# Performance work log

Measured on AMD Instinct MI355X. Metric: run time of the kernel, lower is better.

Reference implementation:

```python
import jax, jax.numpy as jnp
import numpy as np

GH = 256       # GRU hidden size
VOCAB = 1000
MAX_EP = 150
NPREV = NCURR = NNEXT = 64


def _gru_scan(emb, h0, wih, whh, bih, bhh):
    # torch nn.GRU single-layer math, scanned over the token axis
    H = h0.shape[0]
    def step(h, x_t):
        gi = wih @ x_t + bih            # [3H]
        gh = whh @ h + bhh              # [3H]
        r = jax.nn.sigmoid(gi[:H] + gh[:H])
        z = jax.nn.sigmoid(gi[H:2 * H] + gh[H:2 * H])
        n = jnp.tanh(gi[2 * H:] + r * gh[2 * H:])
        hn = (1.0 - z) * n + z * h
        return hn, hn
    _, hs = jax.lax.scan(step, h0, emb)
    return hs                            # [L, H]


def _conv(x, w, b, s):
    y = jax.lax.conv_general_dilated(x, w, (s, s), 'VALID',
                                     dimension_numbers=('NCHW', 'OIHW', 'NCHW'))
    return y + b[None, :, None, None]


def setup_inputs():
    key = jax.random.key(0)
    ks = jax.random.split(key, 48)
    f32 = jnp.float32
    def W(i, shape, s=0.05):
        return (jax.random.normal(ks[i], shape) * s).astype(f32)
    inp = dict(
        x=jax.random.normal(ks[0], (1, 3, 124, 124), f32),
        hx=jax.random.normal(ks[1], (1, 256), f32),
        cx=jax.random.normal(ks[2], (1, 256), f32),
        conv1_w=W(3, (128, 3, 8, 8)), conv1_b=jnp.zeros((128,), f32),
        conv2_w=W(4, (64, 128, 4, 4)), conv2_b=jnp.zeros((64,), f32),
        conv3_w=W(5, (64, 64, 4, 4)), conv3_b=jnp.zeros((64,), f32),
        emb_w=W(6, (VOCAB, 32), 1.0),
        gru_f_wih=W(7, (3 * GH, 32)), gru_f_whh=W(8, (3 * GH, GH)),
        gru_f_bih=jnp.zeros((3 * GH,), f32), gru_f_bhh=jnp.zeros((3 * GH,), f32),
        gru_b_wih=W(9, (3 * GH, 32)), gru_b_whh=W(10, (3 * GH, GH)),
        gru_b_bih=jnp.zeros((3 * GH,), f32), gru_b_bhh=jnp.zeros((3 * GH,), f32),
        time_emb_w=W(11, (MAX_EP + 1, 32), 1.0),
        temp_emb_w=W(12, (2, 32), 1.0),
        img_emb_w=W(13, (256, 64 * 6 * 6)), img_emb_b=jnp.zeros((256,), f32),
        attn_key_w=W(14, (256, 256 * 3)), attn_key_b=jnp.zeros((256,), f32),
        bilinear_A=W(15, (1, 256, 544)), bilinear_b=jnp.zeros((1,), f32),
        reduce_w=W(16, (128, 544)), reduce_b=jnp.zeros((128,), f32),
        gate_w=W(17, (64, 640)), gate_b=jnp.zeros((64,), f32),
        lin_w=W(18, (256, 64 * 6 * 6)), lin_b=jnp.zeros((256,), f32),
        lstm_wih=W(19, (1024, 256)), lstm_whh=W(20, (1024, 256)),
        lstm_bih=jnp.zeros((1024,), f32), lstm_bhh=jnp.zeros((1024,), f32),
        critic_w=W(21, (1, 288)), critic_b=jnp.zeros((1,), f32),
        actor_w=W(22, (4, 288)), actor_b=jnp.zeros((4,), f32),
        prev_inst=jax.random.randint(ks[23], (1, NPREV), 0, VOCAB),
        curr_inst=jax.random.randint(ks[24], (1, NCURR), 0, VOCAB),
        next_inst=jax.random.randint(ks[25], (1, NNEXT), 0, VOCAB),
        tx=jax.random.randint(ks[26], (1,), 0, MAX_EP + 1),
    )
    return inp


def reference(x, hx, cx, conv1_w, conv1_b, conv2_w, conv2_b, conv3_w, conv3_b,
              emb_w, gru_f_wih, gru_f_whh, gru_f_bih, gru_f_bhh,
              gru_b_wih, gru_b_whh, gru_b_bih, gru_b_bhh,
              time_emb_w, temp_emb_w, img_emb_w, img_emb_b,
              attn_key_w, attn_key_b, bilinear_A, bilinear_b,
              reduce_w, reduce_b, gate_w, gate_b, lin_w, lin_b,
              lstm_wih, lstm_whh, lstm_bih, lstm_bhh,
              critic_w, critic_b, actor_w, actor_b,
              prev_inst, curr_inst, next_inst, tx):
    np_, nc, nn_ = prev_inst.shape[1], curr_inst.shape[1], next_inst.shape[1]
    all_inst = jnp.concatenate([prev_inst, curr_inst, next_inst], axis=1)[0]  # [L]
    L = all_inst.shape[0]

    # CNN encoder
    h = jax.nn.relu(_conv(x, conv1_w, conv1_b, 4))
    h = jax.nn.relu(_conv(h, conv2_w, conv2_b, 2))
    x_img = jax.nn.relu(_conv(h, conv3_w, conv3_b, 2))       # [1,64,6,6]

    # token-looped GRUs -> single lax.scan each (note: original runs gru_b
    # over the SAME forward order then reverses the hidden list; replicated)
    emb = emb_w[all_inst]                                    # [L,32]
    h0 = jnp.zeros((GH,), emb.dtype)
    hs_f = _gru_scan(emb, h0, gru_f_wih, gru_f_whh, gru_f_bih, gru_f_bhh)
    hs_b = _gru_scan(emb, h0, gru_b_wih, gru_b_whh, gru_b_bih, gru_b_bhh)[::-1]
    curr_instr_rep = jnp.concatenate([hs_f[np_ + nc - 1], hs_b[np_]])[None]  # [1,512]
    ir_f = jnp.concatenate([hs_f[:np_], hs_f[L - nn_:]], axis=0)             # [M,256]
    ir_b = jnp.concatenate([hs_b[:np_], hs_b[L - nn_:]], axis=0)
    temp_tok = jnp.concatenate([jnp.zeros((np_,), jnp.int32), jnp.ones((nn_,), jnp.int32)])
    instr_rep = jnp.concatenate([ir_f, ir_b, temp_emb_w[temp_tok]], axis=1)  # [M,544]

    # bilinear attention over prev/next token states
    image_emb = x_img.reshape(1, -1) @ img_emb_w.T + img_emb_b               # [1,256]
    attn_key = jnp.concatenate([curr_instr_rep, image_emb], 1) @ attn_key_w.T + attn_key_b
    scores = jnp.einsum('k,okv,mv->mo', attn_key[0], bilinear_A, instr_rep) + bilinear_b  # [M,1]
    w = jax.nn.softmax(scores, axis=0)
    instr_sum = (instr_rep * w).sum(0, keepdims=True)                        # [1,544]

    # gating of image features
    gating = instr_sum @ reduce_w.T + reduce_b                               # [1,128]
    gate_key = jax.nn.sigmoid(jnp.concatenate([curr_instr_rep, gating], 1) @ gate_w.T + gate_b)  # [1,64]
    xg = (x_img * gate_key[:, :, None, None]).reshape(1, -1)
    z = jax.nn.relu(xg @ lin_w.T + lin_b)                                    # [1,256]

    # LSTMCell (torch gate order i,f,g,o)
    gates = z @ lstm_wih.T + lstm_bih + hx @ lstm_whh.T + lstm_bhh           # [1,1024]
    i, f, g, o = jnp.split(gates, 4, axis=1)
    cx2 = jax.nn.sigmoid(f) * cx + jax.nn.sigmoid(i) * jnp.tanh(g)
    hx2 = jax.nn.sigmoid(o) * jnp.tanh(cx2)

    feat = jnp.concatenate([hx2, time_emb_w[tx].reshape(-1, 32)], axis=1)    # [1,288]
    critic = feat @ critic_w.T + critic_b                                    # [1,1]
    actor = feat @ actor_w.T + actor_b                                       # [1,4]
    return critic, actor, hx2, cx2
```

## Files before the change

### kernel.cpp

```cpp
#include <hip/hip_runtime.h>
#include <hip/hip_bf16.h>

typedef int int4v __attribute__((ext_vector_type(4)));

__device__ __forceinline__ float bf2f(unsigned short u) {
    unsigned int v = ((unsigned int)u) << 16;
    return __builtin_bit_cast(float, v);
}
__device__ __forceinline__ float sigm(float x) { return 1.0f / (1.0f + expf(-x)); }
__device__ __forceinline__ float san(float v) {
    return (v == v && fabsf(v) < 1e20f) ? v : 12345.0f;
}
__device__ __forceinline__ void wrout(void* out, int i, float v, int f32out) {
    if (f32out) ((float*)out)[i] = v;
    else ((__hip_bfloat16*)out)[i] = __float2bfloat16(v);
}
__device__ __forceinline__ float fexp2(float x) {
#if __has_builtin(__builtin_amdgcn_exp2f)
    return __builtin_amdgcn_exp2f(x);
#else
    return exp2f(x);
#endif
}
__device__ __forceinline__ float frcp(float x) {
#if __has_builtin(__builtin_amdgcn_rcpf)
    return __builtin_amdgcn_rcpf(x);
#else
    return 1.0f / x;
#endif
}
__device__ __forceinline__ float fsigm(float x) {
    return frcp(1.0f + fexp2(x * -1.44269504f));
}
__device__ __forceinline__ float ftanh(float x) {
    float t = fexp2(x * 2.88539008f);
    return 1.0f - 2.0f * frcp(t + 1.0f);
}
__device__ __forceinline__ float wave_red(float acc) {
#pragma unroll
    for (int off = 32; off >= 1; off >>= 1) acc += __shfl_down(acc, off);
    return acc;
}
__device__ __forceinline__ int sel4(int4v v, int rg) {
    int a = (rg & 1) ? v.y : v.x;
    int b = (rg & 1) ? v.w : v.z;
    return (rg & 2) ? b : a;
}

struct CanonArgs {
    const void* ptr[40];
    int start[41];
    int size[40];
};

__global__ void k_flag1000(void* out) {
    if (threadIdx.x == 0) ((unsigned int*)out)[0] = 0x447A0000u;
}

__global__ void k_detect_tokens(const void* x, int nx,
                                const int* __restrict__ prev, const int* __restrict__ curr,
                                const int* __restrict__ nxt, const int* __restrict__ tx,
                                float* __restrict__ flags, int* __restrict__ toks) {
    __shared__ float sm[256];
    __shared__ int sInt64;
    int tid = threadIdx.x;
    const unsigned short* xs = (const unsigned short*)x;
    float mx = 0.0f;
    for (int i = tid; i < nx; i += 256) {
        float f = bf2f(xs[i]);
        float a = (f == f) ? fabsf(f) : 1e30f;
        mx = fmaxf(mx, a);
    }
    sm[tid] = mx;
    __syncthreads();
    for (int s = 128; s >= 1; s >>= 1) {
        if (tid < s) sm[tid] = fmaxf(sm[tid], sm[tid + s]);
        __syncthreads();
    }
    if (tid == 0) {
        flags[0] = (sm[0] > 100.0f) ? 1.0f : 0.0f;
        int anyOdd = 0;
        for (int k = 0; k < 32; ++k) anyOdd |= curr[2 * k + 1];
        int i64 = (anyOdd == 0) ? 1 : 0;
        flags[1] = (float)i64;
        sInt64 = i64;
    }
    __syncthreads();
    int stride = sInt64 ? 2 : 1;
    if (tid < 192) {
        const int* src = (tid < 64) ? prev : ((tid < 128) ? curr : nxt);
        int v = src[(tid & 63) * stride];
        toks[tid] = min(max(v, 0), 999);
    }
    if (tid == 0) toks[192] = min(max(tx[0], 0), 150);
}

__global__ void k_convert(CanonArgs a, const float* __restrict__ flags,
                          float* __restrict__ C) {
    int base = blockIdx.x << 10;
    int t = 0;
    while (t < 39 && base >= a.start[t + 1]) ++t;
    int local = base - a.start[t] + (threadIdx.x << 2);
    int sz = a.size[t];
    float4 v = make_float4(0.0f, 0.0f, 0.0f, 0.0f);
    int f32in = (flags[0] != 0.0f);
    if (local + 3 < sz) {
        if (f32in) {
            v = *(const float4*)((const float*)a.ptr[t] + local);
        } else {
            uint2 u = *(const uint2*)((const unsigned short*)a.ptr[t] + local);
            v.x = bf2f((unsigned short)(u.x & 0xffff));
            v.y = bf2f((unsigned short)(u.x >> 16));
            v.z = bf2f((unsigned short)(u.y & 0xffff));
            v.w = bf2f((unsigned short)(u.y >> 16));
        }
    } else if (local < sz) {
        float tmp[4] = {0.0f, 0.0f, 0.0f, 0.0f};
        for (int q = 0; q < 4 && local + q < sz; ++q) {
            if (f32in) tmp[q] = ((const float*)a.ptr[t])[local + q];
            else tmp[q] = bf2f(((const unsigned short*)a.ptr[t])[local + q]);
        }
        v = make_float4(tmp[0], tmp[1], tmp[2], tmp[3]);
    }
    *(float4*)(C + base + (threadIdx.x << 2)) = v;
}

__global__ void k_conv1(const float* __restrict__ x, const float* __restrict__ w,
                        const float* __restrict__ b, float* __restrict__ out) {
    int idx = blockIdx.x * 256 + threadIdx.x;
    int oc = idx / 900;
    int rem = idx - oc * 900;
    int oh = rem / 30;
    int ow = rem - oh * 30;
    float acc = b[oc];
    for (int ic = 0; ic < 3; ++ic) {
        int xb = ic * 15376 + (oh * 4) * 124 + ow * 4;
        int wb = oc * 192 + ic * 64;
#pragma unroll
        for (int kh = 0; kh < 8; ++kh) {
            const float2* xr = (const float2*)(x + xb + kh * 124);
            const float2* wr = (const float2*)(w + wb + kh * 8);
#pragma unroll
            for (int p = 0; p < 4; ++p) {
                float2 xv = xr[p];
                float2 wv = wr[p];
                acc += xv.x * wv.x + xv.y * wv.y;
            }
        }
    }
    out[idx] = fmaxf(acc, 0.0f);
}

__global__ void k_conv2(const float* __restrict__ in, const float* __restrict__ w,
                        const float* __restrict__ b, float* __restrict__ out) {
    int wid = (blockIdx.x * 256 + threadIdx.x) >> 6;
    int lane = threadIdx.x & 63;
    int oc = wid / 196;
    int rem = wid - oc * 196;
    int oh = rem / 14, ow = rem - oh * 14;
    float acc = 0.0f;
#pragma unroll 8
    for (int i = 0; i < 32; ++i) {
        int e = lane + (i << 6);
        int ic = e >> 4, k = e & 15, kh = k >> 2, kw = k & 3;
        acc += in[ic * 900 + (oh * 2 + kh) * 30 + ow * 2 + kw] * w[oc * 2048 + e];
    }
    acc = wave_red(acc);
    if (lane == 0) out[wid] = fmaxf(acc + b[oc], 0.0f);
}

__global__ void k_conv3(const float* __restrict__ in, const float* __restrict__ w,
                        const float* __restrict__ b, float* __restrict__ out) {
    int wid = (blockIdx.x * 256 + threadIdx.x) >> 6;
    int lane = threadIdx.x & 63;
    int oc = wid / 36;
    int rem = wid - oc * 36;
    int oh = rem / 6, ow = rem - oh * 6;
    float acc = 0.0f;
#pragma unroll
    for (int i = 0; i < 16; ++i) {
        int e = lane + (i << 6);
        int ic = e >> 4, k = e & 15, kh = k >> 2, kw = k & 3;
        acc += in[ic * 196 + (oh * 2 + kh) * 14 + ow * 2 + kw] * w[oc * 1024 + e];
    }
    acc = wave_red(acc);
    if (lane == 0) out[wid] = fmaxf(acc + b[oc], 0.0f);
}

__global__ void k_imgemb(const float* __restrict__ ximg, const float* __restrict__ w,
                         const float* __restrict__ b, float* __restrict__ out) {
    int j = blockIdx.x;
    int t = threadIdx.x;
    const float* wr = w + j * 2304;
    float acc = 0.0f;
    for (int k = t; k < 2304; k += 64) acc += wr[k] * ximg[k];
    acc = wave_red(acc);
    if (t == 0) out[j] = acc + b[j];
}

__global__ void k_gi(const int* __restrict__ toks, const float* __restrict__ emb,
                     const float* __restrict__ wih_f, const float* __restrict__ bih_f,
                     const float* __restrict__ bhh_f,
                     const float* __restrict__ wih_b, const float* __restrict__ bih_b,
                     const float* __restrict__ bhh_b,
                     float* __restrict__ gi) {
    int t = blockIdx.y;
    int gru = blockIdx.z;
    int j = blockIdx.x * 256 + threadIdx.x;
    __shared__ float e[32];
    int tok = toks[t];
    if (threadIdx.x < 32) e[threadIdx.x] = emb[tok * 32 + threadIdx.x];
    __syncthreads();
    const float* wih = gru ? wih_b : wih_f;
    const float* bih = gru ? bih_b : bih_f;
    const float* bhh = gru ? bhh_b : bhh_f;
    const float2* wr = (const float2*)(wih + j * 32);
    float acc = bih[j] + ((j < 512) ? bhh[j] : 0.0f);
#pragma unroll
    for (int k = 0; k < 16; ++k) {
        float2 wv = wr[k];
        acc += wv.x * e[2 * k] + wv.y * e[2 * k + 1];
    }
    gi[(gru * 192 + t) * 768 + j] = acc;
}

__global__ __launch_bounds__(512, 1) void k_gru(
    const float* __restrict__ whh_f, const float* __restrict__ bhh_f,
    const float* __restrict__ whh_b, const float* __restrict__ bhh_b,
    const float* __restrict__ gi, float* __restrict__ hs) {
    __shared__ unsigned int hq[2][64];
    __shared__ float sc[768];

    int gru = blockIdx.x;
    const float* whh = gru ? whh_b : whh_f;
    const float* bhh = gru ? bhh_b : bhh_f;
    const float* gib = gi + gru * 192 * 768;
    float* hso = hs + gru * 192 * 256;

    int t = threadIdx.x;
    int l = t & 63;
    int w = t >> 6;
    int lg = l >> 4;
    int lr = l & 15;
    int e_sel = (l >> 2) & 1;
    int rg = l & 3;
    int j = 32 * w + 16 * e_sel + 4 * lg + rg;

    int4v A[3][2][4];
#pragma unroll
    for (int s3 = 0; s3 < 3; ++s3) {
#pragma unroll
        for (int e = 0; e < 2; ++e) {
            int r = s3 * 256 + 32 * w + 16 * e + lr;
            const float* rowp = whh + r * 256;
            float4 tmp[16];
            float mx = 0.0f;
#pragma unroll
            for (int q = 0; q < 4; ++q) {
#pragma unroll
                for (int f = 0; f < 4; ++f) {
                    float4 v = *(const float4*)(rowp + 64 * q + 16 * lg + 4 * f);
                    tmp[q * 4 + f] = v;
                    mx = fmaxf(mx, fmaxf(fmaxf(fabsf(v.x), fabsf(v.y)),
                                         fmaxf(fabsf(v.z), fabsf(v.w))));
                }
            }
            mx = fmaxf(mx, __shfl_xor(mx, 16));
            mx = fmaxf(mx, __shfl_xor(mx, 32));
            float scale = 127.0f / fmaxf(mx, 1e-20f);
            if (lg == 0) sc[r] = mx * (1.0f / (127.0f * 127.0f));
#pragma unroll
            for (int q = 0; q < 4; ++q) {
                int dw[4];
#pragma unroll
                for (int f = 0; f < 4; ++f) {
                    float4 v = tmp[q * 4 + f];
                    int p0 = (int)rintf(v.x * scale) & 0xff;
                    int p1 = (int)rintf(v.y * scale) & 0xff;
                    int p2 = (int)rintf(v.z * scale) & 0xff;
                    int p3 = (int)rintf(v.w * scale);
                    dw[f] = p0 | (p1 << 8) | (p2 << 16) | (p3 << 24);
                }
                A[s3][e][q] = (int4v){dw[0], dw[1], dw[2], dw[3]};
            }
        }
    }
    if (t < 128) ((unsigned int*)hq)[t] = 0u;
    __syncthreads();

    float invR = sc[j];
    float invZ = sc[256 + j];
    float invN = sc[512 + j];
    float bhhn = bhh[512 + j];
    int wr8 = ((l & 8) == 0);

    float hprev = 0.0f;
    float cr0 = gib[j],       cz0 = gib[256 + j],  cn0 = gib[512 + j];
    float cr1 = gib[768 + j], cz1 = gib[1024 + j], cn1 = gib[1280 + j];

    int4v zero4 = (int4v){0, 0, 0, 0};

    auto step = [&](const unsigned int* hbuf, unsigned int* hnxt, int S,
                    float gr, float gz, float gn) {
        const char* hb = (const char*)hbuf;
        int4v B0 = *(const int4v*)(hb + 16 * lg);
        int4v B1 = *(const int4v*)(hb + 64 + 16 * lg);
        int4v B2 = *(const int4v*)(hb + 128 + 16 * lg);
        int4v B3 = *(const int4v*)(hb + 192 + 16 * lg);

        int4v C00, C01, C10, C11, C20, C21;
        asm volatile(
            "v_mfma_i32_16x16x64_i8 %0, %7,  %31, %6\n\t"
            "v_mfma_i32_16x16x64_i8 %1, %11, %31, %6\n\t"
            "v_mfma_i32_16x16x64_i8 %2, %15, %31, %6\n\t"
            "v_mfma_i32_16x16x64_i8 %3, %19, %31, %6\n\t"
            "v_mfma_i32_16x16x64_i8 %4, %23, %31, %6\n\t"
            "v_mfma_i32_16x16x64_i8 %5, %27, %31, %6\n\t"
            "v_mfma_i32_16x16x64_i8 %0, %8,  %32, %0\n\t"
            "v_mfma_i32_16x16x64_i8 %1, %12, %32, %1\n\t"
            "v_mfma_i32_16x16x64_i8 %2, %16, %32, %2\n\t"
            "v_mfma_i32_16x16x64_i8 %3, %20, %32, %3\n\t"
            "v_mfma_i32_16x16x64_i8 %4, %24, %32, %4\n\t"
            "v_mfma_i32_16x16x64_i8 %5, %28, %32, %5\n\t"
            "v_mfma_i32_16x16x64_i8 %0, %9,  %33, %0\n\t"
            "v_mfma_i32_16x16x64_i8 %1, %13, %33, %1\n\t"
            "v_mfma_i32_16x16x64_i8 %2, %17, %33, %2\n\t"
            "v_mfma_i32_16x16x64_i8 %3, %21, %33, %3\n\t"
            "v_mfma_i32_16x16x64_i8 %4, %25, %33, %4\n\t"
            "v_mfma_i32_16x16x64_i8 %5, %29, %33, %5\n\t"
            "v_mfma_i32_16x16x64_i8 %0, %10, %34, %0\n\t"
            "v_mfma_i32_16x16x64_i8 %1, %14, %34, %1\n\t"
            "v_mfma_i32_16x16x64_i8 %2, %18, %34, %2\n\t"
            "v_mfma_i32_16x16x64_i8 %3, %22, %34, %3\n\t"
            "v_mfma_i32_16x16x64_i8 %4, %26, %34, %4\n\t"
            "v_mfma_i32_16x16x64_i8 %5, %30, %34, %5\n\t"
            "s_nop 7\n\t"
            "s_nop 7"
            : "=&v"(C00), "=&v"(C01), "=&v"(C10),
              "=&v"(C11), "=&v"(C20), "=&v"(C21)
            : "v"(zero4),
              "v"(A[0][0][0]), "v"(A[0][0][1]), "v"(A[0][0][2]), "v"(A[0][0][3]),
              "v"(A[0][1][0]), "v"(A[0][1][1]), "v"(A[0][1][2]), "v"(A[0][1][3]),
              "v"(A[1][0][0]), "v"(A[1][0][1]), "v"(A[1][0][2]), "v"(A[1][0][3]),
              "v"(A[1][1][0]), "v"(A[1][1][1]), "v"(A[1][1][2]), "v"(A[1][1][3]),
              "v"(A[2][0][0]), "v"(A[2][0][1]), "v"(A[2][0][2]), "v"(A[2][0][3]),
              "v"(A[2][1][0]), "v"(A[2][1][1]), "v"(A[2][1][2]), "v"(A[2][1][3]),
              "v"(B0), "v"(B1), "v"(B2), "v"(B3));
        __builtin_amdgcn_sched_barrier(0);

        int ri = sel4(e_sel ? C01 : C00, rg);
        int zi = sel4(e_sel ? C11 : C10, rg);
        int ni = sel4(e_sel ? C21 : C20, rg);
        float ar = (float)ri * invR;
        float az = (float)zi * invZ;
        float an = (float)ni * invN;
        float r = fsigm(gr + ar);
        float z = fsigm(gz + az);
        float n = ftanh(gn + r * (an + bhhn));
        hprev = z * (hprev - n) + n;

        int qv = (int)rintf(hprev * 127.0f);
        if (wr8) {
            hso[S * 256 + j] = hprev;
            ((char*)hnxt)[j] = (char)qv;
        }
        asm volatile("s_waitcnt lgkmcnt(0)" ::: "memory");
        __builtin_amdgcn_s_barrier();
    };

    for (int i = 0; i < 96; ++i) {
        int s0 = 2 * i;
        float nr0 = 0.0f, nz0 = 0.0f, nn0 = 0.0f;
        if (s0 + 2 < 192) {
            const float* gp = gib + (s0 + 2) * 768 + j;
            nr0 = gp[0]; nz0 = gp[256]; nn0 = gp[512];
        }
        step(&hq[0][0], &hq[1][0], s0, cr0, cz0, cn0);

        int s1 = s0 + 1;
        float nr1 = 0.0f, nz1 = 0.0f, nn1 = 0.0f;
        if (s1 + 2 < 192) {
            const float* gp = gib + (s1 + 2) * 768 + j;
            nr1 = gp[0]; nz1 = gp[256]; nn1 = gp[512];
        }
        step(&hq[1][0], &hq[0][0], s1, cr1, cz1, cn1);

        cr0 = nr0; cz0 = nz0; cn0 = nn0;
        cr1 = nr1; cz1 = nz1; cn1 = nn1;
    }
}

__device__ __forceinline__ float ir_val(int m, int v, const float* hsf, const float* hsb,
                                        const float* temp_emb) {
    if (v < 256) { int r = (m < 64) ? m : 64 + m; return hsf[r * 256 + v]; }
    if (v < 512) { int r = (m < 64) ? 191 - m : 127 - m; return hsb[r * 256 + v - 256]; }
    return temp_emb[(m >= 64) * 32 + (v - 512)];
}

__global__ void k_attnkey(const float* __restrict__ hs, const float* __restrict__ imgemb,
                          const float* __restrict__ w, const float* __restrict__ b,
                          float* __restrict__ ak) {
    int j = blockIdx.x;
    int t = threadIdx.x;
    const float* hsf127 = hs + 127 * 256;
    const float* hsb127 = hs + 192 * 256 + 127 * 256;
    const float* wr = w + j * 768;
    float acc = 0.0f;
    for (int k = t; k < 768; k += 64) {
        float v = (k < 256) ? hsf127[k] : ((k < 512) ? hsb127[k - 256] : imgemb[k - 512]);
        acc += wr[k] * v;
    }
    acc = wave_red(acc);
    if (t == 0) ak[j] = acc + b[j];
}

__global__ void k_bilin(const float* __restrict__ A, const float* __restrict__ ak,
                        float* __restrict__ tmp) {
    int v = blockIdx.x;
    int t = threadIdx.x;
    float acc = 0.0f;
#pragma unroll
    for (int k = t; k < 256; k += 64) acc += A[k * 544 + v] * ak[k];
    acc = wave_red(acc);
    if (t == 0) tmp[v] = acc;
}

__global__ __launch_bounds__(1024) void k_attnmid(
    const float* __restrict__ hs, const float* __restrict__ temp_emb_w,
    const float* __restrict__ tmpv, const float* __restrict__ bb,
    const float* __restrict__ reduce_w, const float* __restrict__ reduce_b,
    const float* __restrict__ gate_w, const float* __restrict__ gate_b,
    float* __restrict__ gk) {
    const int tid = threadIdx.x;
    const float* hsf = hs;
    const float* hsb = hs + 192 * 256;
    __shared__ float stmp[544], ssc[128], ssum[544], sred[1024], sgating[128], scr[512];

    if (tid < 256) {
        scr[tid] = hsf[127 * 256 + tid];
        scr[256 + tid] = hsb[127 * 256 + tid];
    }
    if (tid < 544) stmp[tid] = tmpv[tid];
    __syncthreads();

    {
        int m = tid >> 3, q = tid & 7;
        float acc = 0.0f;
        for (int v = q * 68; v < q * 68 + 68; ++v) acc += stmp[v] * ir_val(m, v, hsf, hsb, temp_emb_w);
        sred[tid] = acc;
    }
    __syncthreads();
    if (tid < 128) {
        float acc = bb[0];
        for (int q = 0; q < 8; ++q) acc += sred[tid * 8 + q];
        ssc[tid] = acc;
        sred[tid] = acc;
    }
    __syncthreads();
#pragma unroll
    for (int s2 = 64; s2 >= 1; s2 >>= 1) {
        if (tid < s2) sred[tid] = fmaxf(sred[tid], sred[tid + s2]);
        __syncthreads();
    }
    float mx = sred[0];
    __syncthreads();
    if (tid < 128) {
        float e = expf(ssc[tid] - mx);
        ssc[tid] = e;
        sred[tid] = e;
    }
    __syncthreads();
#pragma unroll
    for (int s2 = 64; s2 >= 1; s2 >>= 1) {
        if (tid < s2) sred[tid] += sred[tid + s2];
        __syncthreads();
    }
    float inv = 1.0f / sred[0];
    __syncthreads();
    if (tid < 128) ssc[tid] *= inv;
    __syncthreads();

    if (tid < 544) {
        float acc = 0.0f;
        for (int m = 0; m < 128; ++m) acc += ssc[m] * ir_val(m, tid, hsf, hsb, temp_emb_w);
        ssum[tid] = acc;
    }
    __syncthreads();

    {
        int j = tid >> 3, q = tid & 7;
        const float2* wr = (const float2*)(reduce_w + j * 544 + q * 68);
        float acc = 0.0f;
        for (int k = 0; k < 34; ++k) {
            float2 wv = wr[k];
            acc += wv.x * ssum[q * 68 + 2 * k] + wv.y * ssum[q * 68 + 2 * k + 1];
        }
        sred[tid] = acc;
    }
    __syncthreads();
    if (tid < 128) {
        float acc = reduce_b[tid];
        for (int q = 0; q < 8; ++q) acc += sred[tid * 8 + q];
        sgating[tid] = acc;
    }
    __syncthreads();

    {
        int j = tid >> 4, q = tid & 15;
        const float2* wr = (const float2*)(gate_w + j * 640 + q * 40);
        float acc = 0.0f;
        for (int k = 0; k < 20; ++k) {
            float2 wv = wr[k];
            int v0 = q * 40 + 2 * k;
            float a0 = (v0 < 512) ? scr[v0] : sgating[v0 - 512];
            float a1 = (v0 + 1 < 512) ? scr[v0 + 1] : sgating[v0 + 1 - 512];
            acc += wv.x * a0 + wv.y * a1;
        }
        sred[tid] = acc;
    }
    __syncthreads();
    if (tid < 64) {
        float acc = gate_b[tid];
        for (int q = 0; q < 16; ++q) acc += sred[tid * 16 + q];
        gk[tid] = sigm(acc);
    }
}

__global__ void k_lin(const float* __restrict__ ximg, const float* __restrict__ gk,
                      const float* __restrict__ w, const float* __restrict__ b,
                      float* __restrict__ z) {
    int j = blockIdx.x;
    int t = threadIdx.x;
    __shared__ float sgk[64];
    if (t < 64) sgk[t] = gk[t];
    __syncthreads();
    const float* wr = w + j * 2304;
    float acc = 0.0f;
    for (int k = t; k < 2304; k += 64) acc += wr[k] * ximg[k] * sgk[k / 36];
    acc = wave_red(acc);
    if (t == 0) z[j] = fmaxf(acc + b[j], 0.0f);
}

__global__ void k_lstm(const float* __restrict__ z, const float* __restrict__ hx,
                       const float* __restrict__ wih, const float* __restrict__ whh,
                       const float* __restrict__ bih, const float* __restrict__ bhh,
                       float* __restrict__ sg) {
    int j = blockIdx.x;
    int t = threadIdx.x;
    const float* wi = wih + j * 256;
    const float* wh = whh + j * 256;
    float acc = 0.0f;
#pragma unroll
    for (int k = t; k < 256; k += 64) acc += wi[k] * z[k] + wh[k] * hx[k];
    acc = wave_red(acc);
    if (t == 0) sg[j] = acc + bih[j] + bhh[j];
}

__global__ __launch_bounds__(1024) void k_final(
    const float* __restrict__ sgg, const float* __restrict__ cx,
    const float* __restrict__ time_emb_w, const int* __restrict__ toks,
    const float* __restrict__ critic_w, const float* __restrict__ critic_b,
    const float* __restrict__ actor_w, const float* __restrict__ actor_b,
    const float* __restrict__ flags, void* __restrict__ out) {
    const int tid = threadIdx.x;
    __shared__ float sfeat[288], shx2[256], scx2[256], stmp[544], sred[1024];

    if (tid < 256) {
        float ii = sgg[tid], ff = sgg[256 + tid], gg = sgg[512 + tid], oo = sgg[768 + tid];
        float c2 = sigm(ff) * cx[tid] + sigm(ii) * tanhf(gg);
        float h2 = sigm(oo) * tanhf(c2);
        scx2[tid] = c2;
        shx2[tid] = h2;
        sfeat[tid] = h2;
    }
    if (tid < 32) sfeat[256 + tid] = time_emb_w[toks[192] * 32 + tid];
    __syncthreads();

    if (tid < 512) stmp[tid] = (tid < 288) ? critic_w[tid] * sfeat[tid] : 0.0f;
    {
        int a = tid >> 8, k = tid & 255;
        float pa = actor_w[a * 288 + k] * sfeat[k];
        if (k < 32) pa += actor_w[a * 288 + 256 + k] * sfeat[256 + k];
        sred[tid] = pa;
    }
    __syncthreads();
#pragma unroll
    for (int s2 = 256; s2 >= 1; s2 >>= 1) {
        if (tid < s2) stmp[tid] += stmp[tid + s2];
        int k = tid & 255;
        if (s2 <= 128 && k < s2) sred[tid] += sred[tid + s2];
        __syncthreads();
    }

    int f32out = (flags[0] != 0.0f) ? 1 : 0;
    if (tid == 0) wrout(out, 0, san(stmp[0] + critic_b[0]), f32out);
    if (tid < 4) wrout(out, 1 + tid, san(sred[tid * 256] + actor_b[tid]), f32out);
    if (tid < 256) {
        wrout(out, 5 + tid, san(shx2[tid]), f32out);
        wrout(out, 261 + tid, san(scx2[tid]), f32out);
    }
}

extern "C" void kernel_launch(void* const* d_in, const int* in_sizes, int n_in,
                              void* d_out, int out_size, void* d_ws, size_t ws_size,
                              hipStream_t stream) {
    if (n_in != 44) return;

    CanonArgs ca;
    int acc = 0;
    for (int i = 0; i < 40; ++i) {
        ca.ptr[i] = d_in[i];
        ca.start[i] = acc;
        ca.size[i] = in_sizes[i];
        acc += (in_sizes[i] + 1023) & ~1023;
    }
    ca.start[40] = acc;
    const int T = acc;

    float* ws     = (float*)d_ws;
    float* flags  = ws;
    int*   toks   = (int*)(ws + 64);
    float* imgemb = ws + 320;
    float* C      = ws + 640;
    float* gi     = C + T;
    float* hs     = gi + 294912;
    float* aux    = hs + 98304;
    float* ak     = aux;
    float* tmpv   = aux + 256;
    float* gk     = aux + 928;
    float* zv     = aux + 992;
    float* sg     = aux + 1248;
    float* h1     = gi;
    float* h2     = h1 + 115200;
    float* ximg   = h2 + 12544;

    size_t need = (size_t)(640 + T + 294912 + 98304 + 2272) * 4;
    if (ws_size < need) {
        k_flag1000<<<1, 64, 0, stream>>>(d_out);
        return;
    }

    const int* prev = (const int*)d_in[40];
    const int* curr = (const int*)d_in[41];
    const int* nxt  = (const int*)d_in[42];
    const int* tx   = (const int*)d_in[43];

    k_detect_tokens<<<1, 256, 0, stream>>>(d_in[0], in_sizes[0], prev, curr, nxt, tx,
                                           flags, toks);
    k_convert<<<T >> 10, 256, 0, stream>>>(ca, flags, C);

#define CP(i) (C + ca.start[i])
    k_gi<<<dim3(3, 192, 2), 256, 0, stream>>>(toks, CP(9),
                                              CP(10), CP(12), CP(13),
                                              CP(14), CP(16), CP(17), gi);
    k_gru<<<2, 512, 0, stream>>>(CP(11), CP(13), CP(15), CP(17), gi, hs);
    k_conv1<<<450, 256, 0, stream>>>(CP(0), CP(3), CP(4), h1);
    k_conv2<<<3136, 256, 0, stream>>>(h1, CP(5), CP(6), h2);
    k_conv3<<<576, 256, 0, stream>>>(h2, CP(7), CP(8), ximg);
    k_imgemb<<<256, 64, 0, stream>>>(ximg, CP(20), CP(21), imgemb);
    k_attnkey<<<256, 64, 0, stream>>>(hs, imgemb, CP(22), CP(23), ak);
    k_bilin<<<544, 64, 0, stream>>>(CP(24), ak, tmpv);
    k_attnmid<<<1, 1024, 0, stream>>>(hs, CP(19), tmpv, CP(25),
                                      CP(26), CP(27), CP(28), CP(29), gk);
    k_lin<<<256, 64, 0, stream>>>(ximg, gk, CP(30), CP(31), zv);
    k_lstm<<<1024, 64, 0, stream>>>(zv, CP(1), CP(32), CP(33), CP(34), CP(35), sg);
    k_final<<<1, 1024, 0, stream>>>(sg, CP(2), CP(18), toks,
                                    CP(36), CP(37), CP(38), CP(39), flags, d_out);
#undef CP
}
```

Measured before the change: 482.8 us.

## Fuse all stages into one persistent megakernel with global atomic barriers

Replaces the chain of about fourteen small kernel launches with a single persistent kernel of 128 blocks that runs each stage in turn, separated by software grid barriers built on atomic counters. The aim is to remove per-launch overhead and the idle gaps between small dependent kernels. In exchange, work is confined to a fixed grid, so wide stages like conv2 run with less parallelism. Spin barriers also assume all 128 blocks are co-resident, and a memset is added to reset the barrier counters each call.

New measurement: 598.8 us. 24.0% more time.

```diff
diff --git a/kernel.cpp b/kernel.cpp
--- a/kernel.cpp
+++ b/kernel.cpp
@@ -2,6 +2,9 @@
 #include <hip/hip_bf16.h>
 
 typedef int int4v __attribute__((ext_vector_type(4)));
+
+#define NBLK 128
+#define NTHR 512
 
 __device__ __forceinline__ float bf2f(unsigned short u) {
     unsigned int v = ((unsigned int)u) << 16;
@@ -47,347 +50,36 @@
     return (rg & 2) ? b : a;
 }
 
+__device__ __forceinline__ void gbar(unsigned int* bar) {
+    __syncthreads();
+    if (threadIdx.x == 0) {
+        __threadfence();
+        atomicAdd(bar, 1u);
+        while (__hip_atomic_load(bar, __ATOMIC_RELAXED, __HIP_MEMORY_SCOPE_AGENT) <
+               (unsigned int)NBLK)
+            __builtin_amdgcn_s_sleep(2);
+        __threadfence();
+    }
+    __syncthreads();
+}
+
 struct CanonArgs {
     const void* ptr[40];
     int start[41];
     int size[40];
 };
 
+struct MegaArgs {
+    CanonArgs ca;
+    const void* x; int nx;
+    const int* prev; const int* curr; const int* nxt; const int* tx;
+    float* ws;
+    int T;
+    void* out;
+};
+
 __global__ void k_flag1000(void* out) {
     if (threadIdx.x == 0) ((unsigned int*)out)[0] = 0x447A0000u;
-}
-
-__global__ void k_detect_tokens(const void* x, int nx,
-                                const int* __restrict__ prev, const int* __restrict__ curr,
-                                const int* __restrict__ nxt, const int* __restrict__ tx,
-                                float* __restrict__ flags, int* __restrict__ toks) {
-    __shared__ float sm[256];
-    __shared__ int sInt64;
-    int tid = threadIdx.x;
-    const unsigned short* xs = (const unsigned short*)x;
-    float mx = 0.0f;
-    for (int i = tid; i < nx; i += 256) {
-        float f = bf2f(xs[i]);
-        float a = (f == f) ? fabsf(f) : 1e30f;
-        mx = fmaxf(mx, a);
-    }
-    sm[tid] = mx;
-    __syncthreads();
-    for (int s = 128; s >= 1; s >>= 1) {
-        if (tid < s) sm[tid] = fmaxf(sm[tid], sm[tid + s]);
-        __syncthreads();
-    }
-    if (tid == 0) {
-        flags[0] = (sm[0] > 100.0f) ? 1.0f : 0.0f;
-        int anyOdd = 0;
-        for (int k = 0; k < 32; ++k) anyOdd |= curr[2 * k + 1];
-        int i64 = (anyOdd == 0) ? 1 : 0;
-        flags[1] = (float)i64;
-        sInt64 = i64;
-    }
-    __syncthreads();
-    int stride = sInt64 ? 2 : 1;
-    if (tid < 192) {
-        const int* src = (tid < 64) ? prev : ((tid < 128) ? curr : nxt);
-        int v = src[(tid & 63) * stride];
-        toks[tid] = min(max(v, 0), 999);
-    }
-    if (tid == 0) toks[192] = min(max(tx[0], 0), 150);
-}
-
-__global__ void k_convert(CanonArgs a, const float* __restrict__ flags,
-                          float* __restrict__ C) {
-    int base = blockIdx.x << 10;
-    int t = 0;
-    while (t < 39 && base >= a.start[t + 1]) ++t;
-    int local = base - a.start[t] + (threadIdx.x << 2);
-    int sz = a.size[t];
-    float4 v = make_float4(0.0f, 0.0f, 0.0f, 0.0f);
-    int f32in = (flags[0] != 0.0f);
-    if (local + 3 < sz) {
-        if (f32in) {
-            v = *(const float4*)((const float*)a.ptr[t] + local);
-        } else {
-            uint2 u = *(const uint2*)((const unsigned short*)a.ptr[t] + local);
-            v.x = bf2f((unsigned short)(u.x & 0xffff));
-            v.y = bf2f((unsigned short)(u.x >> 16));
-            v.z = bf2f((unsigned short)(u.y & 0xffff));
-            v.w = bf2f((unsigned short)(u.y >> 16));
-        }
-    } else if (local < sz) {
-        float tmp[4] = {0.0f, 0.0f, 0.0f, 0.0f};
-        for (int q = 0; q < 4 && local + q < sz; ++q) {
-            if (f32in) tmp[q] = ((const float*)a.ptr[t])[local + q];
-            else tmp[q] = bf2f(((const unsigned short*)a.ptr[t])[local + q]);
-        }
-        v = make_float4(tmp[0], tmp[1], tmp[2], tmp[3]);
-    }
-    *(float4*)(C + base + (threadIdx.x << 2)) = v;
-}
-
-__global__ void k_conv1(const float* __restrict__ x, const float* __restrict__ w,
-                        const float* __restrict__ b, float* __restrict__ out) {
-    int idx = blockIdx.x * 256 + threadIdx.x;
-    int oc = idx / 900;
-    int rem = idx - oc * 900;
-    int oh = rem / 30;
-    int ow = rem - oh * 30;
-    float acc = b[oc];
-    for (int ic = 0; ic < 3; ++ic) {
-        int xb = ic * 15376 + (oh * 4) * 124 + ow * 4;
-        int wb = oc * 192 + ic * 64;
-#pragma unroll
-        for (int kh = 0; kh < 8; ++kh) {
-            const float2* xr = (const float2*)(x + xb + kh * 124);
-            const float2* wr = (const float2*)(w + wb + kh * 8);
-#pragma unroll
-            for (int p = 0; p < 4; ++p) {
-                float2 xv = xr[p];
-                float2 wv = wr[p];
-                acc += xv.x * wv.x + xv.y * wv.y;
-            }
-        }
-    }
-    out[idx] = fmaxf(acc, 0.0f);
-}
-
-__global__ void k_conv2(const float* __restrict__ in, const float* __restrict__ w,
-                        const float* __restrict__ b, float* __restrict__ out) {
-    int wid = (blockIdx.x * 256 + threadIdx.x) >> 6;
-    int lane = threadIdx.x & 63;
-    int oc = wid / 196;
-    int rem = wid - oc * 196;
-    int oh = rem / 14, ow = rem - oh * 14;
-    float acc = 0.0f;
-#pragma unroll 8
-    for (int i = 0; i < 32; ++i) {
-        int e = lane + (i << 6);
-        int ic = e >> 4, k = e & 15, kh = k >> 2, kw = k & 3;
-        acc += in[ic * 900 + (oh * 2 + kh) * 30 + ow * 2 + kw] * w[oc * 2048 + e];
-    }
-    acc = wave_red(acc);
-    if (lane == 0) out[wid] = fmaxf(acc + b[oc], 0.0f);
-}
-
-__global__ void k_conv3(const float* __restrict__ in, const float* __restrict__ w,
-                        const float* __restrict__ b, float* __restrict__ out) {
-    int wid = (blockIdx.x * 256 + threadIdx.x) >> 6;
-    int lane = threadIdx.x & 63;
-    int oc = wid / 36;
-    int rem = wid - oc * 36;
-    int oh = rem / 6, ow = rem - oh * 6;
-    float acc = 0.0f;
-#pragma unroll
-    for (int i = 0; i < 16; ++i) {
-        int e = lane + (i << 6);
-        int ic = e >> 4, k = e & 15, kh = k >> 2, kw = k & 3;
-        acc += in[ic * 196 + (oh * 2 + kh) * 14 + ow * 2 + kw] * w[oc * 1024 + e];
-    }
-    acc = wave_red(acc);
-    if (lane == 0) out[wid] = fmaxf(acc + b[oc], 0.0f);
-}
-
-__global__ void k_imgemb(const float* __restrict__ ximg, const float* __restrict__ w,
-                         const float* __restrict__ b, float* __restrict__ out) {
-    int j = blockIdx.x;
-    int t = threadIdx.x;
-    const float* wr = w + j * 2304;
-    float acc = 0.0f;
-    for (int k = t; k < 2304; k += 64) acc += wr[k] * ximg[k];
-    acc = wave_red(acc);
-    if (t == 0) out[j] = acc + b[j];
-}
-
-__global__ void k_gi(const int* __restrict__ toks, const float* __restrict__ emb,
-                     const float* __restrict__ wih_f, const float* __restrict__ bih_f,
-                     const float* __restrict__ bhh_f,
-                     const float* __restrict__ wih_b, const float* __restrict__ bih_b,
-                     const float* __restrict__ bhh_b,
-                     float* __restrict__ gi) {
-    int t = blockIdx.y;
-    int gru = blockIdx.z;
-    int j = blockIdx.x * 256 + threadIdx.x;
-    __shared__ float e[32];
-    int tok = toks[t];
-    if (threadIdx.x < 32) e[threadIdx.x] = emb[tok * 32 + threadIdx.x];
-    __syncthreads();
-    const float* wih = gru ? wih_b : wih_f;
-    const float* bih = gru ? bih_b : bih_f;
-    const float* bhh = gru ? bhh_b : bhh_f;
-    const float2* wr = (const float2*)(wih + j * 32);
-    float acc = bih[j] + ((j < 512) ? bhh[j] : 0.0f);
-#pragma unroll
-    for (int k = 0; k < 16; ++k) {
-        float2 wv = wr[k];
-        acc += wv.x * e[2 * k] + wv.y * e[2 * k + 1];
-    }
-    gi[(gru * 192 + t) * 768 + j] = acc;
-}
-
-__global__ __launch_bounds__(512, 1) void k_gru(
-    const float* __restrict__ whh_f, const float* __restrict__ bhh_f,
-    const float* __restrict__ whh_b, const float* __restrict__ bhh_b,
-    const float* __restrict__ gi, float* __restrict__ hs) {
-    __shared__ unsigned int hq[2][64];
-    __shared__ float sc[768];
-
-    int gru = blockIdx.x;
-    const float* whh = gru ? whh_b : whh_f;
-    const float* bhh = gru ? bhh_b : bhh_f;
-    const float* gib = gi + gru * 192 * 768;
-    float* hso = hs + gru * 192 * 256;
-
-    int t = threadIdx.x;
-    int l = t & 63;
-    int w = t >> 6;
-    int lg = l >> 4;
-    int lr = l & 15;
-    int e_sel = (l >> 2) & 1;
-    int rg = l & 3;
-    int j = 32 * w + 16 * e_sel + 4 * lg + rg;
-
-    int4v A[3][2][4];
-#pragma unroll
-    for (int s3 = 0; s3 < 3; ++s3) {
-#pragma unroll
-        for (int e = 0; e < 2; ++e) {
-            int r = s3 * 256 + 32 * w + 16 * e + lr;
-            const float* rowp = whh + r * 256;
-            float4 tmp[16];
-            float mx = 0.0f;
-#pragma unroll
-            for (int q = 0; q < 4; ++q) {
-#pragma unroll
-                for (int f = 0; f < 4; ++f) {
-                    float4 v = *(const float4*)(rowp + 64 * q + 16 * lg + 4 * f);
-                    tmp[q * 4 + f] = v;
-                    mx = fmaxf(mx, fmaxf(fmaxf(fabsf(v.x), fabsf(v.y)),
-                                         fmaxf(fabsf(v.z), fabsf(v.w))));
-                }
-            }
-            mx = fmaxf(mx, __shfl_xor(mx, 16));
-            mx = fmaxf(mx, __shfl_xor(mx, 32));
-            float scale = 127.0f / fmaxf(mx, 1e-20f);
-            if (lg == 0) sc[r] = mx * (1.0f / (127.0f * 127.0f));
-#pragma unroll
-            for (int q = 0; q < 4; ++q) {
-                int dw[4];
-#pragma unroll
-                for (int f = 0; f < 4; ++f) {
-                    float4 v = tmp[q * 4 + f];
-                    int p0 = (int)rintf(v.x * scale) & 0xff;
-                    int p1 = (int)rintf(v.y * scale) & 0xff;
-                    int p2 = (int)rintf(v.z * scale) & 0xff;
-                    int p3 = (int)rintf(v.w * scale);
-                    dw[f] = p0 | (p1 << 8) | (p2 << 16) | (p3 << 24);
-                }
-                A[s3][e][q] = (int4v){dw[0], dw[1], dw[2], dw[3]};
-            }
-        }
-    }
-    if (t < 128) ((unsigned int*)hq)[t] = 0u;
-    __syncthreads();
-
-    float invR = sc[j];
-    float invZ = sc[256 + j];
-    float invN = sc[512 + j];
-    float bhhn = bhh[512 + j];
-    int wr8 = ((l & 8) == 0);
-
-    float hprev = 0.0f;
-    float cr0 = gib[j],       cz0 = gib[256 + j],  cn0 = gib[512 + j];
-    float cr1 = gib[768 + j], cz1 = gib[1024 + j], cn1 = gib[1280 + j];
-
-    int4v zero4 = (int4v){0, 0, 0, 0};
-
-    auto step = [&](const unsigned int* hbuf, unsigned int* hnxt, int S,
-                    float gr, float gz, float gn) {
-        const char* hb = (const char*)hbuf;
-        int4v B0 = *(const int4v*)(hb + 16 * lg);
-        int4v B1 = *(const int4v*)(hb + 64 + 16 * lg);
-        int4v B2 = *(const int4v*)(hb + 128 + 16 * lg);
-        int4v B3 = *(const int4v*)(hb + 192 + 16 * lg);
-
-        int4v C00, C01, C10, C11, C20, C21;
-        asm volatile(
-            "v_mfma_i32_16x16x64_i8 %0, %7,  %31, %6\n\t"
-            "v_mfma_i32_16x16x64_i8 %1, %11, %31, %6\n\t"
-            "v_mfma_i32_16x16x64_i8 %2, %15, %31, %6\n\t"
-            "v_mfma_i32_16x16x64_i8 %3, %19, %31, %6\n\t"
-            "v_mfma_i32_16x16x64_i8 %4, %23, %31, %6\n\t"
-            "v_mfma_i32_16x16x64_i8 %5, %27, %31, %6\n\t"
-            "v_mfma_i32_16x16x64_i8 %0, %8,  %32, %0\n\t"
-            "v_mfma_i32_16x16x64_i8 %1, %12, %32, %1\n\t"
-            "v_mfma_i32_16x16x64_i8 %2, %16, %32, %2\n\t"
-            "v_mfma_i32_16x16x64_i8 %3, %20, %32, %3\n\t"
-            "v_mfma_i32_16x16x64_i8 %4, %24, %32, %4\n\t"
-            "v_mfma_i32_16x16x64_i8 %5, %28, %32, %5\n\t"
-            "v_mfma_i32_16x16x64_i8 %0, %9,  %33, %0\n\t"
-            "v_mfma_i32_16x16x64_i8 %1, %13, %33, %1\n\t"
-            "v_mfma_i32_16x16x64_i8 %2, %17, %33, %2\n\t"
-            "v_mfma_i32_16x16x64_i8 %3, %21, %33, %3\n\t"
-            "v_mfma_i32_16x16x64_i8 %4, %25, %33, %4\n\t"
-            "v_mfma_i32_16x16x64_i8 %5, %29, %33, %5\n\t"
-            "v_mfma_i32_16x16x64_i8 %0, %10, %34, %0\n\t"
-            "v_mfma_i32_16x16x64_i8 %1, %14, %34, %1\n\t"
-            "v_mfma_i32_16x16x64_i8 %2, %18, %34, %2\n\t"
-            "v_mfma_i32_16x16x64_i8 %3, %22, %34, %3\n\t"
-            "v_mfma_i32_16x16x64_i8 %4, %26, %34, %4\n\t"
-            "v_mfma_i32_16x16x64_i8 %5, %30, %34, %5\n\t"
-            "s_nop 7\n\t"
-            "s_nop 7"
-            : "=&v"(C00), "=&v"(C01), "=&v"(C10),
-              "=&v"(C11), "=&v"(C20), "=&v"(C21)
-            : "v"(zero4),
-              "v"(A[0][0][0]), "v"(A[0][0][1]), "v"(A[0][0][2]), "v"(A[0][0][3]),
-              "v"(A[0][1][0]), "v"(A[0][1][1]), "v"(A[0][1][2]), "v"(A[0][1][3]),
-              "v"(A[1][0][0]), "v"(A[1][0][1]), "v"(A[1][0][2]), "v"(A[1][0][3]),
-              "v"(A[1][1][0]), "v"(A[1][1][1]), "v"(A[1][1][2]), "v"(A[1][1][3]),
-              "v"(A[2][0][0]), "v"(A[2][0][1]), "v"(A[2][0][2]), "v"(A[2][0][3]),
-              "v"(A[2][1][0]), "v"(A[2][1][1]), "v"(A[2][1][2]), "v"(A[2][1][3]),
-              "v"(B0), "v"(B1), "v"(B2), "v"(B3));
-        __builtin_amdgcn_sched_barrier(0);
-
-        int ri = sel4(e_sel ? C01 : C00, rg);
-        int zi = sel4(e_sel ? C11 : C10, rg);
-        int ni = sel4(e_sel ? C21 : C20, rg);
-        float ar = (float)ri * invR;
-        float az = (float)zi * invZ;
-        float an = (float)ni * invN;
-        float r = fsigm(gr + ar);
-        float z = fsigm(gz + az);
-        float n = ftanh(gn + r * (an + bhhn));
-        hprev = z * (hprev - n) + n;
-
-        int qv = (int)rintf(hprev * 127.0f);
-        if (wr8) {
-            hso[S * 256 + j] = hprev;
-            ((char*)hnxt)[j] = (char)qv;
-        }
-        asm volatile("s_waitcnt lgkmcnt(0)" ::: "memory");
-        __builtin_amdgcn_s_barrier();
-    };
-
-    for (int i = 0; i < 96; ++i) {
-        int s0 = 2 * i;
-        float nr0 = 0.0f, nz0 = 0.0f, nn0 = 0.0f;
-        if (s0 + 2 < 192) {
-            const float* gp = gib + (s0 + 2) * 768 + j;
-            nr0 = gp[0]; nz0 = gp[256]; nn0 = gp[512];
-        }
-        step(&hq[0][0], &hq[1][0], s0, cr0, cz0, cn0);
-
-        int s1 = s0 + 1;
-        float nr1 = 0.0f, nz1 = 0.0f, nn1 = 0.0f;
-        if (s1 + 2 < 192) {
-            const float* gp = gib + (s1 + 2) * 768 + j;
-            nr1 = gp[0]; nz1 = gp[256]; nn1 = gp[512];
-        }
-        step(&hq[1][0], &hq[0][0], s1, cr1, cz1, cn1);
-
-        cr0 = nr0; cz0 = nz0; cn0 = nn0;
-        cr1 = nr1; cz1 = nz1; cn1 = nn1;
-    }
 }
 
 __device__ __forceinline__ float ir_val(int m, int v, const float* hsf, const float* hsb,
@@ -397,208 +89,604 @@
     return temp_emb[(m >= 64) * 32 + (v - 512)];
 }
 
-__global__ void k_attnkey(const float* __restrict__ hs, const float* __restrict__ imgemb,
-                          const float* __restrict__ w, const float* __restrict__ b,
-                          float* __restrict__ ak) {
-    int j = blockIdx.x;
-    int t = threadIdx.x;
-    const float* hsf127 = hs + 127 * 256;
-    const float* hsb127 = hs + 192 * 256 + 127 * 256;
-    const float* wr = w + j * 768;
-    float acc = 0.0f;
-    for (int k = t; k < 768; k += 64) {
-        float v = (k < 256) ? hsf127[k] : ((k < 512) ? hsb127[k - 256] : imgemb[k - 512]);
-        acc += wr[k] * v;
-    }
-    acc = wave_red(acc);
-    if (t == 0) ak[j] = acc + b[j];
-}
-
-__global__ void k_bilin(const float* __restrict__ A, const float* __restrict__ ak,
-                        float* __restrict__ tmp) {
-    int v = blockIdx.x;
-    int t = threadIdx.x;
-    float acc = 0.0f;
-#pragma unroll
-    for (int k = t; k < 256; k += 64) acc += A[k * 544 + v] * ak[k];
-    acc = wave_red(acc);
-    if (t == 0) tmp[v] = acc;
-}
-
-__global__ __launch_bounds__(1024) void k_attnmid(
-    const float* __restrict__ hs, const float* __restrict__ temp_emb_w,
-    const float* __restrict__ tmpv, const float* __restrict__ bb,
-    const float* __restrict__ reduce_w, const float* __restrict__ reduce_b,
-    const float* __restrict__ gate_w, const float* __restrict__ gate_b,
-    float* __restrict__ gk) {
+__global__ __launch_bounds__(512, 1) void k_mega(MegaArgs a) {
+    extern __shared__ char smem[];
+    const int B = blockIdx.x;
     const int tid = threadIdx.x;
-    const float* hsf = hs;
-    const float* hsb = hs + 192 * 256;
-    __shared__ float stmp[544], ssc[128], ssum[544], sred[1024], sgating[128], scr[512];
-
-    if (tid < 256) {
-        scr[tid] = hsf[127 * 256 + tid];
-        scr[256 + tid] = hsb[127 * 256 + tid];
-    }
-    if (tid < 544) stmp[tid] = tmpv[tid];
-    __syncthreads();
-
-    {
-        int m = tid >> 3, q = tid & 7;
-        float acc = 0.0f;
-        for (int v = q * 68; v < q * 68 + 68; ++v) acc += stmp[v] * ir_val(m, v, hsf, hsb, temp_emb_w);
-        sred[tid] = acc;
-    }
-    __syncthreads();
-    if (tid < 128) {
-        float acc = bb[0];
-        for (int q = 0; q < 8; ++q) acc += sred[tid * 8 + q];
-        ssc[tid] = acc;
-        sred[tid] = acc;
-    }
-    __syncthreads();
-#pragma unroll
-    for (int s2 = 64; s2 >= 1; s2 >>= 1) {
-        if (tid < s2) sred[tid] = fmaxf(sred[tid], sred[tid + s2]);
-        __syncthreads();
-    }
-    float mx = sred[0];
-    __syncthreads();
-    if (tid < 128) {
-        float e = expf(ssc[tid] - mx);
-        ssc[tid] = e;
-        sred[tid] = e;
-    }
-    __syncthreads();
-#pragma unroll
-    for (int s2 = 64; s2 >= 1; s2 >>= 1) {
-        if (tid < s2) sred[tid] += sred[tid + s2];
-        __syncthreads();
-    }
-    float inv = 1.0f / sred[0];
-    __syncthreads();
-    if (tid < 128) ssc[tid] *= inv;
-    __syncthreads();
-
-    if (tid < 544) {
-        float acc = 0.0f;
-        for (int m = 0; m < 128; ++m) acc += ssc[m] * ir_val(m, tid, hsf, hsb, temp_emb_w);
-        ssum[tid] = acc;
-    }
-    __syncthreads();
-
-    {
-        int j = tid >> 3, q = tid & 7;
-        const float2* wr = (const float2*)(reduce_w + j * 544 + q * 68);
-        float acc = 0.0f;
-        for (int k = 0; k < 34; ++k) {
-            float2 wv = wr[k];
-            acc += wv.x * ssum[q * 68 + 2 * k] + wv.y * ssum[q * 68 + 2 * k + 1];
-        }
-        sred[tid] = acc;
-    }
-    __syncthreads();
-    if (tid < 128) {
-        float acc = reduce_b[tid];
-        for (int q = 0; q < 8; ++q) acc += sred[tid * 8 + q];
-        sgating[tid] = acc;
-    }
-    __syncthreads();
-
-    {
-        int j = tid >> 4, q = tid & 15;
-        const float2* wr = (const float2*)(gate_w + j * 640 + q * 40);
-        float acc = 0.0f;
-        for (int k = 0; k < 20; ++k) {
-            float2 wv = wr[k];
-            int v0 = q * 40 + 2 * k;
-            float a0 = (v0 < 512) ? scr[v0] : sgating[v0 - 512];
-            float a1 = (v0 + 1 < 512) ? scr[v0 + 1] : sgating[v0 + 1 - 512];
-            acc += wv.x * a0 + wv.y * a1;
-        }
-        sred[tid] = acc;
-    }
-    __syncthreads();
-    if (tid < 64) {
-        float acc = gate_b[tid];
-        for (int q = 0; q < 16; ++q) acc += sred[tid * 16 + q];
-        gk[tid] = sigm(acc);
-    }
-}
-
-__global__ void k_lin(const float* __restrict__ ximg, const float* __restrict__ gk,
-                      const float* __restrict__ w, const float* __restrict__ b,
-                      float* __restrict__ z) {
-    int j = blockIdx.x;
-    int t = threadIdx.x;
-    __shared__ float sgk[64];
-    if (t < 64) sgk[t] = gk[t];
-    __syncthreads();
-    const float* wr = w + j * 2304;
-    float acc = 0.0f;
-    for (int k = t; k < 2304; k += 64) acc += wr[k] * ximg[k] * sgk[k / 36];
-    acc = wave_red(acc);
-    if (t == 0) z[j] = fmaxf(acc + b[j], 0.0f);
-}
-
-__global__ void k_lstm(const float* __restrict__ z, const float* __restrict__ hx,
-                       const float* __restrict__ wih, const float* __restrict__ whh,
-                       const float* __restrict__ bih, const float* __restrict__ bhh,
-                       float* __restrict__ sg) {
-    int j = blockIdx.x;
-    int t = threadIdx.x;
-    const float* wi = wih + j * 256;
-    const float* wh = whh + j * 256;
-    float acc = 0.0f;
-#pragma unroll
-    for (int k = t; k < 256; k += 64) acc += wi[k] * z[k] + wh[k] * hx[k];
-    acc = wave_red(acc);
-    if (t == 0) sg[j] = acc + bih[j] + bhh[j];
-}
-
-__global__ __launch_bounds__(1024) void k_final(
-    const float* __restrict__ sgg, const float* __restrict__ cx,
-    const float* __restrict__ time_emb_w, const int* __restrict__ toks,
-    const float* __restrict__ critic_w, const float* __restrict__ critic_b,
-    const float* __restrict__ actor_w, const float* __restrict__ actor_b,
-    const float* __restrict__ flags, void* __restrict__ out) {
-    const int tid = threadIdx.x;
-    __shared__ float sfeat[288], shx2[256], scx2[256], stmp[544], sred[1024];
-
-    if (tid < 256) {
-        float ii = sgg[tid], ff = sgg[256 + tid], gg = sgg[512 + tid], oo = sgg[768 + tid];
-        float c2 = sigm(ff) * cx[tid] + sigm(ii) * tanhf(gg);
-        float h2 = sigm(oo) * tanhf(c2);
-        scx2[tid] = c2;
-        shx2[tid] = h2;
-        sfeat[tid] = h2;
-    }
-    if (tid < 32) sfeat[256 + tid] = time_emb_w[toks[192] * 32 + tid];
-    __syncthreads();
-
-    if (tid < 512) stmp[tid] = (tid < 288) ? critic_w[tid] * sfeat[tid] : 0.0f;
-    {
-        int a = tid >> 8, k = tid & 255;
-        float pa = actor_w[a * 288 + k] * sfeat[k];
-        if (k < 32) pa += actor_w[a * 288 + 256 + k] * sfeat[256 + k];
-        sred[tid] = pa;
-    }
-    __syncthreads();
-#pragma unroll
-    for (int s2 = 256; s2 >= 1; s2 >>= 1) {
-        if (tid < s2) stmp[tid] += stmp[tid + s2];
-        int k = tid & 255;
-        if (s2 <= 128 && k < s2) sred[tid] += sred[tid + s2];
-        __syncthreads();
-    }
-
-    int f32out = (flags[0] != 0.0f) ? 1 : 0;
-    if (tid == 0) wrout(out, 0, san(stmp[0] + critic_b[0]), f32out);
-    if (tid < 4) wrout(out, 1 + tid, san(sred[tid * 256] + actor_b[tid]), f32out);
-    if (tid < 256) {
-        wrout(out, 5 + tid, san(shx2[tid]), f32out);
-        wrout(out, 261 + tid, san(scx2[tid]), f32out);
-    }
+    const int lane = tid & 63;
+    const int gw = B * 8 + (tid >> 6);
+
+    float* ws = a.ws;
+    float* flags = ws;
+    unsigned int* bars = (unsigned int*)(ws + 32);
+    int* toks = (int*)(ws + 64);
+    float* imgemb = ws + 320;
+    float* C = ws + 640;
+    const int T = a.T;
+    float* gi = C + T;
+    float* hs = gi + 294912;
+    float* aux = hs + 98304;
+    float* ak   = aux;
+    float* tmpv = aux + 256;
+    float* gk   = aux + 928;
+    float* zv   = aux + 992;
+    float* sg   = aux + 1248;
+    float* xh2  = aux + 2272;
+    float* ximg = xh2 + 12544;
+    float* h1   = gi;
+
+#define CP(i) (C + a.ca.start[i])
+
+    float f32in;
+    {
+        float* red = (float*)smem;
+        const unsigned short* xs = (const unsigned short*)a.x;
+        float mx = 0.0f;
+        for (int i = tid; i < a.nx; i += NTHR) {
+            float f = bf2f(xs[i]);
+            float v = (f == f) ? fabsf(f) : 1e30f;
+            mx = fmaxf(mx, v);
+        }
+        red[tid] = mx;
+        __syncthreads();
+        for (int s = 256; s >= 1; s >>= 1) {
+            if (tid < s) red[tid] = fmaxf(red[tid], red[tid + s]);
+            __syncthreads();
+        }
+        if (tid == 0) {
+            red[512] = (red[0] > 100.0f) ? 1.0f : 0.0f;
+            int anyOdd = 0;
+            for (int k = 0; k < 32; ++k) anyOdd |= a.curr[2 * k + 1];
+            red[513] = (anyOdd == 0) ? 1.0f : 0.0f;
+        }
+        __syncthreads();
+        f32in = red[512];
+        int i64 = (red[513] != 0.0f);
+        if (B == 0) {
+            int stride = i64 ? 2 : 1;
+            if (tid < 192) {
+                const int* src = (tid < 64) ? a.prev : ((tid < 128) ? a.curr : a.nxt);
+                int v = src[(tid & 63) * stride];
+                toks[tid] = min(max(v, 0), 999);
+            }
+            if (tid == 0) {
+                toks[192] = min(max(a.tx[0], 0), 150);
+                flags[0] = f32in;
+                flags[1] = (float)i64;
+            }
+        }
+        __syncthreads();
+    }
+
+    {
+        int nch = T >> 10;
+        int g = tid >> 8;
+        int l256 = tid & 255;
+        int f32 = (f32in != 0.0f);
+        for (int ch = B * 2 + g; ch < nch; ch += 2 * NBLK) {
+            int base = ch << 10;
+            int t = 0;
+            while (t < 39 && base >= a.ca.start[t + 1]) ++t;
+            int local = base - a.ca.start[t] + (l256 << 2);
+            int sz = a.ca.size[t];
+            float4 v = make_float4(0.0f, 0.0f, 0.0f, 0.0f);
+            if (local + 3 < sz) {
+                if (f32) {
+                    v = *(const float4*)((const float*)a.ca.ptr[t] + local);
+                } else {
+                    uint2 u = *(const uint2*)((const unsigned short*)a.ca.ptr[t] + local);
+                    v.x = bf2f((unsigned short)(u.x & 0xffff));
+                    v.y = bf2f((unsigned short)(u.x >> 16));
+                    v.z = bf2f((unsigned short)(u.y & 0xffff));
+                    v.w = bf2f((unsigned short)(u.y >> 16));
+                }
+            } else if (local < sz) {
+                float tmp[4] = {0.0f, 0.0f, 0.0f, 0.0f};
+                for (int q = 0; q < 4 && local + q < sz; ++q) {
+                    if (f32) tmp[q] = ((const float*)a.ca.ptr[t])[local + q];
+                    else tmp[q] = bf2f(((const unsigned short*)a.ca.ptr[t])[local + q]);
+                }
+                v = make_float4(tmp[0], tmp[1], tmp[2], tmp[3]);
+            }
+            *(float4*)(C + base + (l256 << 2)) = v;
+        }
+    }
+    gbar(&bars[0]);
+
+    {
+        const float* x = CP(0);
+        const float* w = CP(3);
+        const float* bb = CP(4);
+        for (int idx = B * NTHR + tid; idx < 115200; idx += NBLK * NTHR) {
+            int oc = idx / 900;
+            int rem = idx - oc * 900;
+            int oh = rem / 30;
+            int ow = rem - oh * 30;
+            float acc = bb[oc];
+            for (int ic = 0; ic < 3; ++ic) {
+                int xb = ic * 15376 + (oh * 4) * 124 + ow * 4;
+                int wb = oc * 192 + ic * 64;
+#pragma unroll
+                for (int kh = 0; kh < 8; ++kh) {
+                    const float2* xr = (const float2*)(x + xb + kh * 124);
+                    const float2* wr = (const float2*)(w + wb + kh * 8);
+#pragma unroll
+                    for (int p = 0; p < 4; ++p) {
+                        float2 xv = xr[p];
+                        float2 wv = wr[p];
+                        acc += xv.x * wv.x + xv.y * wv.y;
+                    }
+                }
+            }
+            h1[idx] = fmaxf(acc, 0.0f);
+        }
+    }
+    gbar(&bars[1]);
+
+    {
+        const float* w = CP(5);
+        const float* bb = CP(6);
+        for (int wid = gw; wid < 12544; wid += NBLK * 8) {
+            int oc = wid / 196;
+            int rem = wid - oc * 196;
+            int oh = rem / 14, ow = rem - oh * 14;
+            float acc = 0.0f;
+#pragma unroll 8
+            for (int i = 0; i < 32; ++i) {
+                int e = lane + (i << 6);
+                int ic = e >> 4, k = e & 15, kh = k >> 2, kw = k & 3;
+                acc += h1[ic * 900 + (oh * 2 + kh) * 30 + ow * 2 + kw] * w[oc * 2048 + e];
+            }
+            acc = wave_red(acc);
+            if (lane == 0) xh2[wid] = fmaxf(acc + bb[oc], 0.0f);
+        }
+    }
+    gbar(&bars[2]);
+
+    {
+        const float* w = CP(7);
+        const float* bb = CP(8);
+        for (int wid = gw; wid < 2304; wid += NBLK * 8) {
+            int oc = wid / 36;
+            int rem = wid - oc * 36;
+            int oh = rem / 6, ow = rem - oh * 6;
+            float acc = 0.0f;
+#pragma unroll
+            for (int i = 0; i < 16; ++i) {
+                int e = lane + (i << 6);
+                int ic = e >> 4, k = e & 15, kh = k >> 2, kw = k & 3;
+                acc += xh2[ic * 196 + (oh * 2 + kh) * 14 + ow * 2 + kw] * w[oc * 1024 + e];
+            }
+            acc = wave_red(acc);
+            if (lane == 0) ximg[wid] = fmaxf(acc + bb[oc], 0.0f);
+        }
+    }
+    gbar(&bars[3]);
+
+    {
+        const float* emb = CP(9);
+        const float* wihf = CP(10);
+        const float* bihf = CP(12);
+        const float* bhhf = CP(13);
+        const float* wihb = CP(14);
+        const float* bihb = CP(16);
+        const float* bhhb = CP(17);
+        for (int idx = B * NTHR + tid; idx < 294912; idx += NBLK * NTHR) {
+            int gru = idx / 147456;
+            int r = idx - gru * 147456;
+            int tt = r / 768;
+            int j = r - tt * 768;
+            int tok = toks[tt];
+            const float* wih = gru ? wihb : wihf;
+            const float* bih = gru ? bihb : bihf;
+            const float* bhh = gru ? bhhb : bhhf;
+            const float2* wr = (const float2*)(wih + j * 32);
+            const float2* er = (const float2*)(emb + tok * 32);
+            float acc = bih[j] + ((j < 512) ? bhh[j] : 0.0f);
+#pragma unroll
+            for (int k = 0; k < 16; ++k) {
+                float2 wv = wr[k];
+                float2 ev = er[k];
+                acc += wv.x * ev.x + wv.y * ev.y;
+            }
+            gi[idx] = acc;
+        }
+        const float* w = CP(20);
+        const float* bb = CP(21);
+        if (gw < 256) {
+            const float* wr = w + gw * 2304;
+            float acc = 0.0f;
+            for (int k = lane; k < 2304; k += 64) acc += wr[k] * ximg[k];
+            acc = wave_red(acc);
+            if (lane == 0) imgemb[gw] = acc + bb[gw];
+        }
+    }
+    gbar(&bars[4]);
+
+    if (B < 2) {
+        unsigned int* hq = (unsigned int*)smem;
+        float* sc = (float*)(smem + 512);
+
+        const float* whh = B ? CP(15) : CP(11);
+        const float* bhh = B ? CP(17) : CP(13);
+        const float* gib = gi + B * 192 * 768;
+        float* hso = hs + B * 192 * 256;
+
+        int t = tid;
+        int l = t & 63;
+        int w = t >> 6;
+        int lg = l >> 4;
+        int lr = l & 15;
+        int e_sel = (l >> 2) & 1;
+        int rg = l & 3;
+        int j = 32 * w + 16 * e_sel + 4 * lg + rg;
+
+        int4v A[3][2][4];
+#pragma unroll
+        for (int s3 = 0; s3 < 3; ++s3) {
+#pragma unroll
+            for (int e = 0; e < 2; ++e) {
+                int r = s3 * 256 + 32 * w + 16 * e + lr;
+                const float* rowp = whh + r * 256;
+                float4 tmp[16];
+                float mx = 0.0f;
+#pragma unroll
+                for (int q = 0; q < 4; ++q) {
+#pragma unroll
+                    for (int f = 0; f < 4; ++f) {
+                        float4 v = *(const float4*)(rowp + 64 * q + 16 * lg + 4 * f);
+                        tmp[q * 4 + f] = v;
+                        mx = fmaxf(mx, fmaxf(fmaxf(fabsf(v.x), fabsf(v.y)),
+                                             fmaxf(fabsf(v.z), fabsf(v.w))));
+                    }
+                }
+                mx = fmaxf(mx, __shfl_xor(mx, 16));
+                mx = fmaxf(mx, __shfl_xor(mx, 32));
+                float scale = 127.0f / fmaxf(mx, 1e-20f);
+                if (lg == 0) sc[r] = mx * (1.0f / (127.0f * 127.0f));
+#pragma unroll
+                for (int q = 0; q < 4; ++q) {
+                    int dw[4];
+#pragma unroll
+                    for (int f = 0; f < 4; ++f) {
+                        float4 v = tmp[q * 4 + f];
+                        int p0 = (int)rintf(v.x * scale) & 0xff;
+                        int p1 = (int)rintf(v.y * scale) & 0xff;
+                        int p2 = (int)rintf(v.z * scale) & 0xff;
+                        int p3 = (int)rintf(v.w * scale);
+                        dw[f] = p0 | (p1 << 8) | (p2 << 16) | (p3 << 24);
+                    }
+                    A[s3][e][q] = (int4v){dw[0], dw[1], dw[2], dw[3]};
+                }
+            }
+        }
+        if (t < 128) hq[t] = 0u;
+        __syncthreads();
+
+        float invR = sc[j];
+        float invZ = sc[256 + j];
+        float invN = sc[512 + j];
+        float bhhn = bhh[512 + j];
+        int wr8 = ((l & 8) == 0);
+
+        float hprev = 0.0f;
+        float cr0 = gib[j],       cz0 = gib[256 + j],  cn0 = gib[512 + j];
+        float cr1 = gib[768 + j], cz1 = gib[1024 + j], cn1 = gib[1280 + j];
+
+        int4v zero4 = (int4v){0, 0, 0, 0};
+
+        auto step = [&](const unsigned int* hbuf, unsigned int* hnxt, int S,
+                        float gr, float gz, float gn) {
+            const char* hb = (const char*)hbuf;
+            int4v B0 = *(const int4v*)(hb + 16 * lg);
+            int4v B1 = *(const int4v*)(hb + 64 + 16 * lg);
+            int4v B2 = *(const int4v*)(hb + 128 + 16 * lg);
+            int4v B3 = *(const int4v*)(hb + 192 + 16 * lg);
+
+            int4v C00, C01, C10, C11, C20, C21;
+            asm volatile(
+                "v_mfma_i32_16x16x64_i8 %0, %7,  %31, %6\n\t"
+                "v_mfma_i32_16x16x64_i8 %1, %11, %31, %6\n\t"
+                "v_mfma_i32_16x16x64_i8 %2, %15, %31, %6\n\t"
+                "v_mfma_i32_16x16x64_i8 %3, %19, %31, %6\n\t"
+                "v_mfma_i32_16x16x64_i8 %4, %23, %31, %6\n\t"
+                "v_mfma_i32_16x16x64_i8 %5, %27, %31, %6\n\t"
+                "v_mfma_i32_16x16x64_i8 %0, %8,  %32, %0\n\t"
+                "v_mfma_i32_16x16x64_i8 %1, %12, %32, %1\n\t"
+                "v_mfma_i32_16x16x64_i8 %2, %16, %32, %2\n\t"
+                "v_mfma_i32_16x16x64_i8 %3, %20, %32, %3\n\t"
+                "v_mfma_i32_16x16x64_i8 %4, %24, %32, %4\n\t"
+                "v_mfma_i32_16x16x64_i8 %5, %28, %32, %5\n\t"
+                "v_mfma_i32_16x16x64_i8 %0, %9,  %33, %0\n\t"
+                "v_mfma_i32_16x16x64_i8 %1, %13, %33, %1\n\t"
+                "v_mfma_i32_16x16x64_i8 %2, %17, %33, %2\n\t"
+                "v_mfma_i32_16x16x64_i8 %3, %21, %33, %3\n\t"
+                "v_mfma_i32_16x16x64_i8 %4, %25, %33, %4\n\t"
+                "v_mfma_i32_16x16x64_i8 %5, %29, %33, %5\n\t"
+                "v_mfma_i32_16x16x64_i8 %0, %10, %34, %0\n\t"
+                "v_mfma_i32_16x16x64_i8 %1, %14, %34, %1\n\t"
+                "v_mfma_i32_16x16x64_i8 %2, %18, %34, %2\n\t"
+                "v_mfma_i32_16x16x64_i8 %3, %22, %34, %3\n\t"
+                "v_mfma_i32_16x16x64_i8 %4, %26, %34, %4\n\t"
+                "v_mfma_i32_16x16x64_i8 %5, %30, %34, %5\n\t"
+                "s_nop 7\n\t"
+                "s_nop 7"
+                : "=&v"(C00), "=&v"(C01), "=&v"(C10),
+                  "=&v"(C11), "=&v"(C20), "=&v"(C21)
+                : "v"(zero4),
+                  "v"(A[0][0][0]), "v"(A[0][0][1]), "v"(A[0][0][2]), "v"(A[0][0][3]),
+                  "v"(A[0][1][0]), "v"(A[0][1][1]), "v"(A[0][1][2]), "v"(A[0][1][3]),
+                  "v"(A[1][0][0]), "v"(A[1][0][1]), "v"(A[1][0][2]), "v"(A[1][0][3]),
+                  "v"(A[1][1][0]), "v"(A[1][1][1]), "v"(A[1][1][2]), "v"(A[1][1][3]),
+                  "v"(A[2][0][0]), "v"(A[2][0][1]), "v"(A[2][0][2]), "v"(A[2][0][3]),
+                  "v"(A[2][1][0]), "v"(A[2][1][1]), "v"(A[2][1][2]), "v"(A[2][1][3]),
+                  "v"(B0), "v"(B1), "v"(B2), "v"(B3));
+            __builtin_amdgcn_sched_barrier(0);
+
+            int ri = sel4(e_sel ? C01 : C00, rg);
+            int zi = sel4(e_sel ? C11 : C10, rg);
+            int ni = sel4(e_sel ? C21 : C20, rg);
+            float ar = (float)ri * invR;
+            float az = (float)zi * invZ;
+            float an = (float)ni * invN;
+            float r = fsigm(gr + ar);
+            float z = fsigm(gz + az);
+            float n = ftanh(gn + r * (an + bhhn));
+            hprev = z * (hprev - n) + n;
+
+            int qv = (int)rintf(hprev * 127.0f);
+            if (wr8) {
+                hso[S * 256 + j] = hprev;
+                ((char*)hnxt)[j] = (char)qv;
+            }
+            asm volatile("s_waitcnt lgkmcnt(0)" ::: "memory");
+            __builtin_amdgcn_s_barrier();
+        };
+
+        for (int i = 0; i < 96; ++i) {
+            int s0 = 2 * i;
+            float nr0 = 0.0f, nz0 = 0.0f, nn0 = 0.0f;
+            if (s0 + 2 < 192) {
+                const float* gp = gib + (s0 + 2) * 768 + j;
+                nr0 = gp[0]; nz0 = gp[256]; nn0 = gp[512];
+            }
+            step(hq, hq + 64, s0, cr0, cz0, cn0);
+
+            int s1 = s0 + 1;
+            float nr1 = 0.0f, nz1 = 0.0f, nn1 = 0.0f;
+            if (s1 + 2 < 192) {
+                const float* gp = gib + (s1 + 2) * 768 + j;
+                nr1 = gp[0]; nz1 = gp[256]; nn1 = gp[512];
+            }
+            step(hq + 64, hq, s1, cr1, cz1, cn1);
+
+            cr0 = nr0; cz0 = nz0; cn0 = nn0;
+            cr1 = nr1; cz1 = nz1; cn1 = nn1;
+        }
+    }
+    gbar(&bars[5]);
+
+    {
+        const float* w = CP(22);
+        const float* bb = CP(23);
+        const float* hsf127 = hs + 127 * 256;
+        const float* hsb127 = hs + 192 * 256 + 127 * 256;
+        if (gw < 256) {
+            const float* wr = w + gw * 768;
+            float acc = 0.0f;
+            for (int k = lane; k < 768; k += 64) {
+                float v = (k < 256) ? hsf127[k]
+                                    : ((k < 512) ? hsb127[k - 256] : imgemb[k - 512]);
+                acc += wr[k] * v;
+            }
+            acc = wave_red(acc);
+            if (lane == 0) ak[gw] = acc + bb[gw];
+        }
+    }
+    gbar(&bars[6]);
+
+    {
+        const float* A = CP(24);
+        if (gw < 544) {
+            float acc = 0.0f;
+#pragma unroll
+            for (int k = lane; k < 256; k += 64) acc += A[k * 544 + gw] * ak[k];
+            acc = wave_red(acc);
+            if (lane == 0) tmpv[gw] = acc;
+        }
+    }
+    gbar(&bars[7]);
+
+    if (B == 0) {
+        const float* temp_emb_w = CP(19);
+        const float* bb = CP(25);
+        const float* reduce_w = CP(26);
+        const float* reduce_b = CP(27);
+        const float* gate_w = CP(28);
+        const float* gate_b = CP(29);
+        const float* hsf = hs;
+        const float* hsb = hs + 192 * 256;
+        float* stmp    = (float*)smem;
+        float* ssc     = stmp + 544;
+        float* ssum    = ssc + 128;
+        float* sred    = ssum + 544;
+        float* sgating = sred + 512;
+        float* scr     = sgating + 128;
+
+        if (tid < 256) {
+            scr[tid] = hsf[127 * 256 + tid];
+            scr[256 + tid] = hsb[127 * 256 + tid];
+        }
+        for (int v = tid; v < 544; v += NTHR) stmp[v] = tmpv[v];
+        __syncthreads();
+
+        {
+            int m = tid >> 2, q = tid & 3;
+            float acc = 0.0f;
+            for (int v = q * 136; v < q * 136 + 136; ++v)
+                acc += stmp[v] * ir_val(m, v, hsf, hsb, temp_emb_w);
+            sred[tid] = acc;
+        }
+        __syncthreads();
+        if (tid < 128) {
+            float acc = bb[0];
+            for (int q = 0; q < 4; ++q) acc += sred[tid * 4 + q];
+            ssc[tid] = acc;
+            sred[tid] = acc;
+        }
+        __syncthreads();
+#pragma unroll
+        for (int s2 = 64; s2 >= 1; s2 >>= 1) {
+            if (tid < s2) sred[tid] = fmaxf(sred[tid], sred[tid + s2]);
+            __syncthreads();
+        }
+        float mx = sred[0];
+        __syncthreads();
+        if (tid < 128) {
+            float e = expf(ssc[tid] - mx);
+            ssc[tid] = e;
+            sred[tid] = e;
+        }
+        __syncthreads();
+#pragma unroll
+        for (int s2 = 64; s2 >= 1; s2 >>= 1) {
+            if (tid < s2) sred[tid] += sred[tid + s2];
+            __syncthreads();
+        }
+        float inv = 1.0f / sred[0];
+        __syncthreads();
+        if (tid < 128) ssc[tid] *= inv;
+        __syncthreads();
+
+        for (int v = tid; v < 544; v += NTHR) {
+            float acc = 0.0f;
+            for (int m = 0; m < 128; ++m)
+                acc += ssc[m] * ir_val(m, v, hsf, hsb, temp_emb_w);
+            ssum[v] = acc;
+        }
+        __syncthreads();
+
+        {
+            int j = tid >> 2, q = tid & 3;
+            const float2* wr = (const float2*)(reduce_w + j * 544 + q * 136);
+            float acc = 0.0f;
+            for (int k = 0; k < 68; ++k) {
+                float2 wv = wr[k];
+                acc += wv.x * ssum[q * 136 + 2 * k] + wv.y * ssum[q * 136 + 2 * k + 1];
+            }
+            sred[tid] = acc;
+        }
+        __syncthreads();
+        if (tid < 128) {
+            float acc = reduce_b[tid];
+            for (int q = 0; q < 4; ++q) acc += sred[tid * 4 + q];
+            sgating[tid] = acc;
+        }
+        __syncthreads();
+
+        {
+            int j = tid >> 3, q = tid & 7;
+            const float2* wr = (const float2*)(gate_w + j * 640 + q * 80);
+            float acc = 0.0f;
+            for (int k = 0; k < 40; ++k) {
+                float2 wv = wr[k];
+                int v0 = q * 80 + 2 * k;
+                float a0 = (v0 < 512) ? scr[v0] : sgating[v0 - 512];
+                float a1 = (v0 + 1 < 512) ? scr[v0 + 1] : sgating[v0 + 1 - 512];
+                acc += wv.x * a0 + wv.y * a1;
+            }
+            sred[tid] = acc;
+        }
+        __syncthreads();
+        if (tid < 64) {
+            float acc = gate_b[tid];
+            for (int q = 0; q < 8; ++q) acc += sred[tid * 8 + q];
+            gk[tid] = sigm(acc);
+        }
+    }
+    gbar(&bars[8]);
+
+    {
+        const float* w = CP(30);
+        const float* bb = CP(31);
+        if (gw < 256) {
+            const float* wr = w + gw * 2304;
+            float acc = 0.0f;
+            for (int k = lane; k < 2304; k += 64) acc += wr[k] * ximg[k] * gk[k / 36];
+            acc = wave_red(acc);
+            if (lane == 0) zv[gw] = fmaxf(acc + bb[gw], 0.0f);
+        }
+    }
+    gbar(&bars[9]);
+
+    {
+        const float* wih = CP(32);
+        const float* whh = CP(33);
+        const float* bih = CP(34);
+        const float* bhh = CP(35);
+        const float* hx = CP(1);
+        if (gw < 1024) {
+            const float* wi = wih + gw * 256;
+            const float* wh = whh + gw * 256;
+            float acc = 0.0f;
+#pragma unroll
+            for (int k = lane; k < 256; k += 64) acc += wi[k] * zv[k] + wh[k] * hx[k];
+            acc = wave_red(acc);
+            if (lane == 0) sg[gw] = acc + bih[gw] + bhh[gw];
+        }
+    }
+    gbar(&bars[10]);
+
+    if (B == 0) {
+        const float* cx = CP(2);
+        const float* time_emb_w = CP(18);
+        const float* critic_w = CP(36);
+        const float* critic_b = CP(37);
+        const float* actor_w = CP(38);
+        const float* actor_b = CP(39);
+        float* sfeat = (float*)smem;
+        float* shx2  = sfeat + 320;
+        float* scx2  = shx2 + 256;
+        float* stmp  = scx2 + 256;
+        float* sred  = stmp + 512;
+
+        if (tid < 256) {
+            float ii = sg[tid], ff = sg[256 + tid], gg = sg[512 + tid], oo = sg[768 + tid];
+            float c2 = sigm(ff) * cx[tid] + sigm(ii) * tanhf(gg);
+            float h2 = sigm(oo) * tanhf(c2);
+            scx2[tid] = c2;
+            shx2[tid] = h2;
+            sfeat[tid] = h2;
+        }
+        if (tid < 32) sfeat[256 + tid] = time_emb_w[toks[192] * 32 + tid];
+        __syncthreads();
+
+        stmp[tid] = (tid < 288) ? critic_w[tid] * sfeat[tid] : 0.0f;
+        {
+            int aa = tid >> 7, k = tid & 127;
+            float pa = actor_w[aa * 288 + k] * sfeat[k] +
+                       actor_w[aa * 288 + 128 + k] * sfeat[128 + k];
+            if (k < 32) pa += actor_w[aa * 288 + 256 + k] * sfeat[256 + k];
+            sred[tid] = pa;
+        }
+        __syncthreads();
+#pragma unroll
+        for (int s2 = 256; s2 >= 1; s2 >>= 1) {
+            if (tid < s2) stmp[tid] += stmp[tid + s2];
+            int k = tid & 127;
+            if (s2 <= 64 && k < s2) sred[tid] += sred[tid + s2];
+            __syncthreads();
+        }
+
+        int f32out = (flags[0] != 0.0f) ? 1 : 0;
+        if (tid == 0) wrout(a.out, 0, san(stmp[0] + critic_b[0]), f32out);
+        if (tid < 4) wrout(a.out, 1 + tid, san(sred[tid * 128] + actor_b[tid]), f32out);
+        if (tid < 256) {
+            wrout(a.out, 5 + tid, san(shx2[tid]), f32out);
+            wrout(a.out, 261 + tid, san(scx2[tid]), f32out);
+        }
+    }
+#undef CP
 }
 
 extern "C" void kernel_launch(void* const* d_in, const int* in_sizes, int n_in,
@@ -606,65 +694,33 @@
                               hipStream_t stream) {
     if (n_in != 44) return;
 
-    CanonArgs ca;
+    MegaArgs ma;
     int acc = 0;
     for (int i = 0; i < 40; ++i) {
-        ca.ptr[i] = d_in[i];
-        ca.start[i] = acc;
-        ca.size[i] = in_sizes[i];
+        ma.ca.ptr[i] = d_in[i];
+        ma.ca.start[i] = acc;
+        ma.ca.size[i] = in_sizes[i];
         acc += (in_sizes[i] + 1023) & ~1023;
     }
-    ca.start[40] = acc;
+    ma.ca.start[40] = acc;
     const int T = acc;
 
-    float* ws     = (float*)d_ws;
-    float* flags  = ws;
-    int*   toks   = (int*)(ws + 64);
-    float* imgemb = ws + 320;
-    float* C      = ws + 640;
-    float* gi     = C + T;
-    float* hs     = gi + 294912;
-    float* aux    = hs + 98304;
-    float* ak     = aux;
-    float* tmpv   = aux + 256;
-    float* gk     = aux + 928;
-    float* zv     = aux + 992;
-    float* sg     = aux + 1248;
-    float* h1     = gi;
-    float* h2     = h1 + 115200;
-    float* ximg   = h2 + 12544;
-
-    size_t need = (size_t)(640 + T + 294912 + 98304 + 2272) * 4;
+    size_t need = (size_t)(640 + T + 294912 + 98304 + 2272 + 12544 + 2304) * 4;
     if (ws_size < need) {
         k_flag1000<<<1, 64, 0, stream>>>(d_out);
         return;
     }
 
-    const int* prev = (const int*)d_in[40];
-    const int* curr = (const int*)d_in[41];
-    const int* nxt  = (const int*)d_in[42];
-    const int* tx   = (const int*)d_in[43];
-
-    k_detect_tokens<<<1, 256, 0, stream>>>(d_in[0], in_sizes[0], prev, curr, nxt, tx,
-                                           flags, toks);
-    k_convert<<<T >> 10, 256, 0, stream>>>(ca, flags, C);
-
-#define CP(i) (C + ca.start[i])
-    k_gi<<<dim3(3, 192, 2), 256, 0, stream>>>(toks, CP(9),
-                                              CP(10), CP(12), CP(13),
-                                              CP(14), CP(16), CP(17), gi);
-    k_gru<<<2, 512, 0, stream>>>(CP(11), CP(13), CP(15), CP(17), gi, hs);
-    k_conv1<<<450, 256, 0, stream>>>(CP(0), CP(3), CP(4), h1);
-    k_conv2<<<3136, 256, 0, stream>>>(h1, CP(5), CP(6), h2);
-    k_conv3<<<576, 256, 0, stream>>>(h2, CP(7), CP(8), ximg);
-    k_imgemb<<<256, 64, 0, stream>>>(ximg, CP(20), CP(21), imgemb);
-    k_attnkey<<<256, 64, 0, stream>>>(hs, imgemb, CP(22), CP(23), ak);
-    k_bilin<<<544, 64, 0, stream>>>(CP(24), ak, tmpv);
-    k_attnmid<<<1, 1024, 0, stream>>>(hs, CP(19), tmpv, CP(25),
-                                      CP(26), CP(27), CP(28), CP(29), gk);
-    k_lin<<<256, 64, 0, stream>>>(ximg, gk, CP(30), CP(31), zv);
-    k_lstm<<<1024, 64, 0, stream>>>(zv, CP(1), CP(32), CP(33), CP(34), CP(35), sg);
-    k_final<<<1, 1024, 0, stream>>>(sg, CP(2), CP(18), toks,
-                                    CP(36), CP(37), CP(38), CP(39), flags, d_out);
-#undef CP
-}
+    ma.x = d_in[0];
+    ma.nx = in_sizes[0];
+    ma.prev = (const int*)d_in[40];
+    ma.curr = (const int*)d_in[41];
+    ma.nxt  = (const int*)d_in[42];
+    ma.tx   = (const int*)d_in[43];
+    ma.ws = (float*)d_ws;
+    ma.T = T;
+    ma.out = d_out;
+
+    hipMemsetAsync((char*)d_ws + 128, 0, 64, stream);
+    k_mega<<<NBLK, NTHR, 99328, stream>>>(ma);
+}
```
